# Performance work log

Measured on AMD Instinct MI355X. Metric: run time of the kernel, lower is better.

Reference implementation:

```python
import math
import jax, jax.numpy as jnp
import numpy as np

B, S, D, H = 4, 2048, 1024, 16
DH = D // H  # 64


def setup_inputs() -> dict:
    key = jax.random.key(0)
    k1, k2, k3 = jax.random.split(key, 3)
    x = jax.random.normal(k1, (B, S, D), dtype=jnp.float32)
    W_qkv = jax.random.normal(k2, (D, 3 * D), dtype=jnp.float32) * (1.0 / math.sqrt(D))
    b_qkv = jax.random.normal(k3, (3 * D,), dtype=jnp.float32) * 0.02
    return {"x": x, "W_qkv": W_qkv, "b_qkv": b_qkv}


def reference(x, W_qkv, b_qkv):
    b, s, d = x.shape
    qkv = x @ W_qkv + b_qkv                       # [B,S,3D]
    # Faithful to torch: view(B,S,H,3,D_h) -> interleaved per-head q/k/v split
    qkv = qkv.reshape(b, s, H, 3, DH)
    q = jnp.transpose(qkv[:, :, :, 0, :], (0, 2, 1, 3))  # [B,H,S,DH]
    k = jnp.transpose(qkv[:, :, :, 1, :], (0, 2, 1, 3))
    v = jnp.transpose(qkv[:, :, :, 2, :], (0, 2, 1, 3))
    scores = jnp.einsum('bhsd,bhtd->bhst', q, k) / math.sqrt(DH)  # [B,H,S,S]
    causal = jnp.triu(jnp.ones((s, s), dtype=bool), k=1)
    scores = jnp.where(causal, -jnp.inf, scores)
    weights = jax.nn.softmax(scores, axis=-1)
    # dropout is identity in eval/reference mode
    context = jnp.einsum('bhst,bhtd->bhsd', weights, v)  # [B,H,S,DH]
    return jnp.transpose(context, (0, 2, 1, 3)).reshape(b, s, d)
```

## Files before the change

kernel.cpp:

```cpp
#include <hip/hip_runtime.h>
#include <hip/hip_bf16.h>

#define Bz 4
#define Sz 2048
#define Dz 1024
#define Hz 16
#define DHz 64
#define Mz (Bz*Sz)
#define N3z (3*Dz)
#define Kz Dz

typedef short s16x8 __attribute__((ext_vector_type(8)));
typedef float f32x4 __attribute__((ext_vector_type(4)));
typedef unsigned short u16;

__device__ __forceinline__ u16 f2b(float f) {
  union { float f; unsigned u; } v; v.f = f;
  unsigned r = v.u + 0x7FFFu + ((v.u >> 16) & 1u);
  return (u16)(r >> 16);
}

__device__ __forceinline__ unsigned cvt_pk_bf16(float lo, float hi) {
  unsigned r;
  asm("v_cvt_pk_bf16_f32 %0, %1, %2" : "=v"(r) : "v"(lo), "v"(hi));
  return r;
}

__global__ __launch_bounds__(256) void cvt_x(const float* __restrict__ x,
                                             u16* __restrict__ xb) {
  int i = (blockIdx.x * 256 + threadIdx.x) * 4;
  float4 v = *reinterpret_cast<const float4*>(x + i);
  ushort4 o;
  o.x = f2b(v.x); o.y = f2b(v.y); o.z = f2b(v.z); o.w = f2b(v.w);
  *reinterpret_cast<ushort4*>(xb + i) = o;
}

__global__ __launch_bounds__(256) void transpose_w(const float* __restrict__ W,
                                                   u16* __restrict__ Wt) {
  __shared__ u16 t[32][33];
  int nb = blockIdx.x;
  int kb = blockIdx.y;
  int tx = threadIdx.x, ty = threadIdx.y;
#pragma unroll
  for (int j = 0; j < 4; ++j) {
    int k = kb * 32 + ty + j * 8;
    t[ty + j * 8][tx] = f2b(W[(size_t)k * N3z + nb * 32 + tx]);
  }
  __syncthreads();
#pragma unroll
  for (int j = 0; j < 4; ++j) {
    int n = nb * 32 + ty + j * 8;
    Wt[(size_t)n * Kz + kb * 32 + tx] = t[tx][ty + j * 8];
  }
}

#define BM 128
#define BN 128
#define BKs 64
#define QSCALE (0.125f * 1.44269504088896f)

__global__ __launch_bounds__(256) void qkv_gemm(
    const u16* __restrict__ A, const u16* __restrict__ Bt,
    const float* __restrict__ bias,
    u16* __restrict__ Qo, u16* __restrict__ Ko, u16* __restrict__ Vt) {
  __shared__ alignas(16) u16 As[BM * BKs];
  __shared__ alignas(16) u16 Bs[BN * BKs];
  const int tid = threadIdx.x;
  const int wid = tid >> 6, lane = tid & 63;
  const int wr = wid >> 1, wc = wid & 1;
  const int g = lane >> 4, lq = lane & 15;

  const int id = blockIdx.x + gridDim.x * blockIdx.y;
  const int xc = id & 7, rr = id >> 3;
  const int bx = xc * 8 + (rr & 7);
  const int by = rr >> 3;
  const int brow = bx * BM;
  const int bcol = by * BN;

  const int soff = (((lane & 7) ^ (lane >> 3))) * 8;

  f32x4 acc[4][4] = {};

  for (int kt = 0; kt < Kz; kt += BKs) {
#pragma unroll
    for (int c = 0; c < 4; ++c) {
      int row = (wid * 4 + c) * 8 + (lane >> 3);
      const u16* ga = A + (size_t)(brow + row) * Kz + kt + soff;
      __builtin_amdgcn_global_load_lds(
          (const __attribute__((address_space(1))) void*)ga,
          (__attribute__((address_space(3))) void*)&As[(wid * 4 + c) * 512],
          16, 0, 0);
      const u16* gb = Bt + (size_t)(bcol + row) * Kz + kt + soff;
      __builtin_amdgcn_global_load_lds(
          (const __attribute__((address_space(1))) void*)gb,
          (__attribute__((address_space(3))) void*)&Bs[(wid * 4 + c) * 512],
          16, 0, 0);
    }
    __syncthreads();

#pragma unroll
    for (int ks = 0; ks < 2; ++ks) {
      s16x8 af[4], bfr[4];
#pragma unroll
      for (int i = 0; i < 4; ++i) {
        int rowa = wr * 64 + i * 16 + lq;
        int rowb = wc * 64 + i * 16 + lq;
        int sl = ((ks * 4 + g) ^ (lq & 7)) << 4;
        af[i]  = *reinterpret_cast<const s16x8*>((const char*)As + rowa * 128 + sl);
        bfr[i] = *reinterpret_cast<const s16x8*>((const char*)Bs + rowb * 128 + sl);
      }
#pragma unroll
      for (int mi = 0; mi < 4; ++mi)
#pragma unroll
        for (int ni = 0; ni < 4; ++ni)
          acc[mi][ni] = __builtin_amdgcn_mfma_f32_16x16x32_bf16(af[mi], bfr[ni], acc[mi][ni], 0, 0, 0);
    }
    __syncthreads();
  }

#pragma unroll
  for (int ni = 0; ni < 4; ++ni) {
    int gcol = bcol + wc * 64 + ni * 16 + lq;
    int h = gcol / 192;
    int rem = gcol - h * 192;
    int tt = rem >> 6;
    int dh = rem & 63;
    float bv = bias[gcol];
    u16* dst = (tt == 0) ? Qo : (tt == 1) ? Ko : Vt;
    float scale = (tt == 0) ? QSCALE : 1.0f;
    bool isv = (tt == 2);
#pragma unroll
    for (int mi = 0; mi < 4; ++mi) {
#pragma unroll
      for (int r = 0; r < 4; ++r) {
        int grow = brow + wr * 64 + mi * 16 + g * 4 + r;
        int bb = grow >> 11;
        int ss = grow & 2047;
        float v = (acc[mi][ni][r] + bv) * scale;
        size_t off = isv ? ((((size_t)bb * Hz + h) * DHz + dh) * Sz + ss)
                         : ((((size_t)bb * Hz + h) * Sz + ss) * DHz + dh);
        dst[off] = f2b(v);
      }
    }
  }
}

__device__ __forceinline__ void attn_tile(
    const char* KsC, const char* VsC, int kv0, int q0w, int qrow,
    int g, int lq, int p, int cb, int sEven, int sOdd,
    const s16x8& qf0, const s16x8& qf1,
    f32x4 (&o)[4], float& m1, float& l1) {
  if (kv0 > q0w + 15) return;

  f32x4 z[4];
#pragma unroll
  for (int f = 0; f < 4; ++f) {
    int row = f * 16 + lq;
    s16x8 kb0 = *reinterpret_cast<const s16x8*>(KsC + row * 128 + ((g ^ (row & 7)) << 4));
    s16x8 kb1 = *reinterpret_cast<const s16x8*>(KsC + row * 128 + (((g + 4) ^ (row & 7)) << 4));
    f32x4 zz = {0.f, 0.f, 0.f, 0.f};
    zz = __builtin_amdgcn_mfma_f32_16x16x32_bf16(kb0, qf0, zz, 0, 0, 0);
    zz = __builtin_amdgcn_mfma_f32_16x16x32_bf16(kb1, qf1, zz, 0, 0, 0);
    z[f] = zz;
  }

  if (kv0 + 63 > q0w) {
#pragma unroll
    for (int f = 0; f < 4; ++f)
#pragma unroll
      for (int r = 0; r < 4; ++r) {
        int key = kv0 + f * 16 + g * 4 + r;
        if (key > qrow) z[f][r] = -1e30f;
      }
  }

  float pm = z[0][0];
#pragma unroll
  for (int f = 0; f < 4; ++f)
#pragma unroll
    for (int r = 0; r < 4; ++r) pm = fmaxf(pm, z[f][r]);
  pm = fmaxf(pm, __shfl_xor(pm, 16));
  pm = fmaxf(pm, __shfl_xor(pm, 32));

  if (!__all(pm <= m1 + 8.0f)) {
    float mn = fmaxf(m1, pm);
    float a = exp2f(m1 - mn);
    m1 = mn;
    l1 *= a;
    float a0 = __shfl(a, 4 * g + 0);
    float a1 = __shfl(a, 4 * g + 1);
    float a2 = __shfl(a, 4 * g + 2);
    float a3 = __shfl(a, 4 * g + 3);
#pragma unroll
    for (int ni = 0; ni < 4; ++ni) {
      o[ni][0] *= a0; o[ni][1] *= a1; o[ni][2] *= a2; o[ni][3] *= a3;
    }
  }

  float s = 0.f;
  unsigned w[4][2];
#pragma unroll
  for (int f = 0; f < 4; ++f) {
    float p0 = exp2f(z[f][0] - m1);
    float p1 = exp2f(z[f][1] - m1);
    float p2 = exp2f(z[f][2] - m1);
    float p3 = exp2f(z[f][3] - m1);
    s += (p0 + p1) + (p2 + p3);
    w[f][0] = cvt_pk_bf16(p0, p1);
    w[f][1] = cvt_pk_bf16(p2, p3);
  }
  s += __shfl_xor(s, 16);
  s += __shfl_xor(s, 32);
  l1 += s;

  int e0 = __shfl((int)(p ? w[1][0] : w[0][0]), sEven);
  int o0 = __shfl((int)(p ? w[0][0] : w[1][0]), sOdd);
  int e1 = __shfl((int)(p ? w[1][1] : w[0][1]), sEven);
  int o1 = __shfl((int)(p ? w[0][1] : w[1][1]), sOdd);
  int e2 = __shfl((int)(p ? w[3][0] : w[2][0]), sEven);
  int o2 = __shfl((int)(p ? w[2][0] : w[3][0]), sOdd);
  int e3 = __shfl((int)(p ? w[3][1] : w[2][1]), sEven);
  int o3 = __shfl((int)(p ? w[2][1] : w[3][1]), sOdd);
  union { int i[4]; s16x8 v; } A0, A1;
  A0.i[0] = cb ? o0 : e0;
  A0.i[2] = cb ? e0 : o0;
  A0.i[1] = cb ? o1 : e1;
  A0.i[3] = cb ? e1 : o1;
  A1.i[0] = cb ? o2 : e2;
  A1.i[2] = cb ? e2 : o2;
  A1.i[1] = cb ? o3 : e3;
  A1.i[3] = cb ? e3 : o3;

#pragma unroll
  for (int ni = 0; ni < 4; ++ni) {
    int row = ni * 16 + lq;
    s16x8 vb0 = *reinterpret_cast<const s16x8*>(VsC + row * 128 + ((g ^ (row & 7)) << 4));
    s16x8 vb1 = *reinterpret_cast<const s16x8*>(VsC + row * 128 + (((g + 4) ^ (row & 7)) << 4));
    o[ni] = __builtin_amdgcn_mfma_f32_16x16x32_bf16(A0.v, vb0, o[ni], 0, 0, 0);
    o[ni] = __builtin_amdgcn_mfma_f32_16x16x32_bf16(A1.v, vb1, o[ni], 0, 0, 0);
  }
}

__global__ __launch_bounds__(512, 4) void attn_kernel(
    const u16* __restrict__ Qg, const u16* __restrict__ Kg,
    const u16* __restrict__ Vtg, float* __restrict__ out) {
  __shared__ alignas(16) u16 Ks[2][64 * 64];
  __shared__ alignas(16) u16 Vs[2][64 * 64];

  const int tid = threadIdx.x;
  const int wid = tid >> 6, lane = tid & 63;
  const int g = lane >> 4, lq = lane & 15;

  const int id = blockIdx.x + 8 * blockIdx.y;
  const int xc = id & 7, rr = id >> 3;
  const int bh = xc * 8 + (rr & 7);
  const int qp = rr >> 3;

  const size_t base = (size_t)bh * Sz * DHz;
  const int b = bh >> 4, h = bh & 15;

  const int krow = tid >> 3;
  const int sswz = ((tid & 7) ^ (krow & 7)) * 8;

  const int p = g & 1;
  const int cb = g >> 1;
  const int sA = 32 * (g & 1) + lq;
  const int sB = sA + 16;
  const int sEven = cb ? sB : sA;
  const int sOdd  = cb ? sA : sB;

  const int qtA = qp, qtB = 15 - qp;
  const int q0wA = qtA * 128 + wid * 16;
  const int q0wB = qtB * 128 + wid * 16;
  const int qrowA = q0wA + lq, qrowB = q0wB + lq;
  const int ntA = 2 * qtA + 2, ntB = 2 * qtB + 2;

  s16x8 qfA0 = *reinterpret_cast<const s16x8*>(Qg + base + (size_t)qrowA * DHz + g * 8);
  s16x8 qfA1 = *reinterpret_cast<const s16x8*>(Qg + base + (size_t)qrowA * DHz + g * 8 + 32);
  s16x8 qfB0 = *reinterpret_cast<const s16x8*>(Qg + base + (size_t)qrowB * DHz + g * 8);
  s16x8 qfB1 = *reinterpret_cast<const s16x8*>(Qg + base + (size_t)qrowB * DHz + g * 8 + 32);

  f32x4 oA[4] = {}, oB[4] = {};
  float mA = -1e30f, lA = 0.f, mB = -1e30f, lB = 0.f;

  {
    const u16* gk = Kg + base + (size_t)krow * DHz + sswz;
    __builtin_amdgcn_global_load_lds(
        (const __attribute__((address_space(1))) void*)gk,
        (__attribute__((address_space(3))) void*)&Ks[0][wid * 512], 16, 0, 0);
    const u16* gv = Vtg + base + (size_t)krow * Sz + sswz;
    __builtin_amdgcn_global_load_lds(
        (const __attribute__((address_space(1))) void*)gv,
        (__attribute__((address_space(3))) void*)&Vs[0][wid * 512], 16, 0, 0);
  }
  __syncthreads();

  int cur = 0;
  for (int t = 0; t < ntB; ++t) {
    const int kv0 = t * 64;

    if (t + 1 < ntB) {
      const int nv0 = kv0 + 64;
      const u16* gk = Kg + base + (size_t)(nv0 + krow) * DHz + sswz;
      __builtin_amdgcn_global_load_lds(
          (const __attribute__((address_space(1))) void*)gk,
          (__attribute__((address_space(3))) void*)&Ks[cur ^ 1][wid * 512], 16, 0, 0);
      const u16* gv = Vtg + base + (size_t)krow * Sz + nv0 + sswz;
      __builtin_amdgcn_global_load_lds(
          (const __attribute__((address_space(1))) void*)gv,
          (__attribute__((address_space(3))) void*)&Vs[cur ^ 1][wid * 512], 16, 0, 0);
    }

    const char* KsC = (const char*)Ks[cur];
    const char* VsC = (const char*)Vs[cur];

    attn_tile(KsC, VsC, kv0, q0wB, qrowB, g, lq, p, cb, sEven, sOdd,
              qfB0, qfB1, oB, mB, lB);
    if (t < ntA)
      attn_tile(KsC, VsC, kv0, q0wA, qrowA, g, lq, p, cb, sEven, sOdd,
                qfA0, qfA1, oA, mA, lA);

    __syncthreads();
    cur ^= 1;
  }

#pragma unroll
  for (int half = 0; half < 2; ++half) {
    const int q0w = half ? q0wB : q0wA;
    f32x4* o = half ? oB : oA;
    float l1 = half ? lB : lA;
    float lr0 = __shfl(l1, 4 * g + 0);
    float lr1 = __shfl(l1, 4 * g + 1);
    float lr2 = __shfl(l1, 4 * g + 2);
    float lr3 = __shfl(l1, 4 * g + 3);
    float inv[4] = {1.0f / lr0, 1.0f / lr1, 1.0f / lr2, 1.0f / lr3};
#pragma unroll
    for (int r = 0; r < 4; ++r) {
      int s = q0w + g * 4 + r;
      float* op = out + (((size_t)b * Sz + s) * Hz + h) * DHz;
#pragma unroll
      for (int ni = 0; ni < 4; ++ni)
        op[ni * 16 + lq] = o[ni][r] * inv[r];
    }
  }
}

extern "C" void kernel_launch(void* const* d_in, const int* in_sizes, int n_in,
                              void* d_out, int out_size, void* d_ws, size_t ws_size,
                              hipStream_t stream) {
  const float* x    = (const float*)d_in[0];
  const float* W    = (const float*)d_in[1];
  const float* bias = (const float*)d_in[2];
  float* out = (float*)d_out;

  char* ws = (char*)d_ws;
  u16* xb = (u16*)(ws);
  u16* wt = (u16*)(ws + 16777216);
  u16* Qb = (u16*)(ws + 23068672);
  u16* Kb = (u16*)(ws + 39845888);
  u16* Vtb = (u16*)(ws + 56623104);

  cvt_x<<<8192, 256, 0, stream>>>(x, xb);
  transpose_w<<<dim3(96, 32), dim3(32, 8), 0, stream>>>(W, wt);
  qkv_gemm<<<dim3(Mz / BM, N3z / BN), 256, 0, stream>>>(xb, wt, bias, Qb, Kb, Vtb);
  attn_kernel<<<dim3(8, Bz * Hz), 512, 0, stream>>>(Qb, Kb, Vtb, out);
}
```

Before: 242.4 us.

## Fuse prep kernels, shrink GEMM K-tile, stage 128-key attention tiles

Merges the x conversion and W transpose kernels into one launch to save a launch. In the QKV GEMM it halves the K-tile to 32, drops the XOR LDS swizzle and the block-index remap, and uses plain row-major shared tiles. This may bring LDS bank conflicts and worse L2 locality. Attention now loads 128 keys per stage with double-buffered pairs of 64-key buffers, halving barrier count. It also unrolls the row-max reduction, but the A query tile is now processed on every stage even when fully masked, which adds redundant work.

New measurement: 234.8 us. -3.1%, faster.

```diff
diff --git a/kernel.cpp b/kernel.cpp
--- a/kernel.cpp
+++ b/kernel.cpp
@@ -26,37 +26,41 @@
   return r;
 }
 
-__global__ __launch_bounds__(256) void cvt_x(const float* __restrict__ x,
-                                             u16* __restrict__ xb) {
-  int i = (blockIdx.x * 256 + threadIdx.x) * 4;
-  float4 v = *reinterpret_cast<const float4*>(x + i);
-  ushort4 o;
-  o.x = f2b(v.x); o.y = f2b(v.y); o.z = f2b(v.z); o.w = f2b(v.w);
-  *reinterpret_cast<ushort4*>(xb + i) = o;
-}
-
-__global__ __launch_bounds__(256) void transpose_w(const float* __restrict__ W,
-                                                   u16* __restrict__ Wt) {
+__global__ __launch_bounds__(256) void prep(const float* __restrict__ x,
+                                            u16* __restrict__ xb,
+                                            const float* __restrict__ W,
+                                            u16* __restrict__ Wt) {
   __shared__ u16 t[32][33];
-  int nb = blockIdx.x;
-  int kb = blockIdx.y;
-  int tx = threadIdx.x, ty = threadIdx.y;
-#pragma unroll
-  for (int j = 0; j < 4; ++j) {
-    int k = kb * 32 + ty + j * 8;
-    t[ty + j * 8][tx] = f2b(W[(size_t)k * N3z + nb * 32 + tx]);
-  }
-  __syncthreads();
-#pragma unroll
-  for (int j = 0; j < 4; ++j) {
-    int n = nb * 32 + ty + j * 8;
-    Wt[(size_t)n * Kz + kb * 32 + tx] = t[tx][ty + j * 8];
+  const int bid = blockIdx.x;
+  const int tid = threadIdx.x;
+  if (bid < 8192) {
+    int i = (bid * 256 + tid) * 4;
+    float4 v = *reinterpret_cast<const float4*>(x + i);
+    ushort4 o;
+    o.x = f2b(v.x); o.y = f2b(v.y); o.z = f2b(v.z); o.w = f2b(v.w);
+    *reinterpret_cast<ushort4*>(xb + i) = o;
+  } else {
+    int id2 = bid - 8192;
+    int nb = id2 % 96;
+    int kb = id2 / 96;
+    int tx = tid & 31, ty = tid >> 5;
+#pragma unroll
+    for (int j = 0; j < 4; ++j) {
+      int k = kb * 32 + ty + j * 8;
+      t[ty + j * 8][tx] = f2b(W[(size_t)k * N3z + nb * 32 + tx]);
+    }
+    __syncthreads();
+#pragma unroll
+    for (int j = 0; j < 4; ++j) {
+      int n = nb * 32 + ty + j * 8;
+      Wt[(size_t)n * Kz + kb * 32 + tx] = t[tx][ty + j * 8];
+    }
   }
 }
 
 #define BM 128
 #define BN 128
-#define BKs 64
+#define BKs 32
 #define QSCALE (0.125f * 1.44269504088896f)
 
 __global__ __launch_bounds__(256) void qkv_gemm(
@@ -69,52 +73,40 @@
   const int wid = tid >> 6, lane = tid & 63;
   const int wr = wid >> 1, wc = wid & 1;
   const int g = lane >> 4, lq = lane & 15;
-
-  const int id = blockIdx.x + gridDim.x * blockIdx.y;
-  const int xc = id & 7, rr = id >> 3;
-  const int bx = xc * 8 + (rr & 7);
-  const int by = rr >> 3;
-  const int brow = bx * BM;
-  const int bcol = by * BN;
-
-  const int soff = (((lane & 7) ^ (lane >> 3))) * 8;
+  const int brow = blockIdx.x * BM;
+  const int bcol = blockIdx.y * BN;
 
   f32x4 acc[4][4] = {};
 
   for (int kt = 0; kt < Kz; kt += BKs) {
 #pragma unroll
-    for (int c = 0; c < 4; ++c) {
-      int row = (wid * 4 + c) * 8 + (lane >> 3);
-      const u16* ga = A + (size_t)(brow + row) * Kz + kt + soff;
+    for (int c = 0; c < 2; ++c) {
+      int row = (wid * 2 + c) * 16 + (lane >> 2);
+      int off = (lane & 3) * 8;
+      const u16* ga = A + (size_t)(brow + row) * Kz + kt + off;
       __builtin_amdgcn_global_load_lds(
           (const __attribute__((address_space(1))) void*)ga,
-          (__attribute__((address_space(3))) void*)&As[(wid * 4 + c) * 512],
+          (__attribute__((address_space(3))) void*)&As[(wid * 2 + c) * 512],
           16, 0, 0);
-      const u16* gb = Bt + (size_t)(bcol + row) * Kz + kt + soff;
+      const u16* gb = Bt + (size_t)(bcol + row) * Kz + kt + off;
       __builtin_amdgcn_global_load_lds(
           (const __attribute__((address_space(1))) void*)gb,
-          (__attribute__((address_space(3))) void*)&Bs[(wid * 4 + c) * 512],
+          (__attribute__((address_space(3))) void*)&Bs[(wid * 2 + c) * 512],
           16, 0, 0);
     }
     __syncthreads();
 
-#pragma unroll
-    for (int ks = 0; ks < 2; ++ks) {
-      s16x8 af[4], bfr[4];
-#pragma unroll
-      for (int i = 0; i < 4; ++i) {
-        int rowa = wr * 64 + i * 16 + lq;
-        int rowb = wc * 64 + i * 16 + lq;
-        int sl = ((ks * 4 + g) ^ (lq & 7)) << 4;
-        af[i]  = *reinterpret_cast<const s16x8*>((const char*)As + rowa * 128 + sl);
-        bfr[i] = *reinterpret_cast<const s16x8*>((const char*)Bs + rowb * 128 + sl);
-      }
-#pragma unroll
-      for (int mi = 0; mi < 4; ++mi)
-#pragma unroll
-        for (int ni = 0; ni < 4; ++ni)
-          acc[mi][ni] = __builtin_amdgcn_mfma_f32_16x16x32_bf16(af[mi], bfr[ni], acc[mi][ni], 0, 0, 0);
-    }
+    s16x8 af[4], bfr[4];
+#pragma unroll
+    for (int i = 0; i < 4; ++i) {
+      af[i]  = *reinterpret_cast<const s16x8*>(&As[(wr * 64 + i * 16 + lq) * BKs + g * 8]);
+      bfr[i] = *reinterpret_cast<const s16x8*>(&Bs[(wc * 64 + i * 16 + lq) * BKs + g * 8]);
+    }
+#pragma unroll
+    for (int mi = 0; mi < 4; ++mi)
+#pragma unroll
+      for (int ni = 0; ni < 4; ++ni)
+        acc[mi][ni] = __builtin_amdgcn_mfma_f32_16x16x32_bf16(af[mi], bfr[ni], acc[mi][ni], 0, 0, 0);
     __syncthreads();
   }
 
@@ -174,11 +166,15 @@
       }
   }
 
-  float pm = z[0][0];
-#pragma unroll
-  for (int f = 0; f < 4; ++f)
-#pragma unroll
-    for (int r = 0; r < 4; ++r) pm = fmaxf(pm, z[f][r]);
+  float pm;
+  pm = fmaxf(fmaxf(z[0][0], z[0][1]), z[0][2]);
+  pm = fmaxf(fmaxf(pm, z[0][3]), z[1][0]);
+  pm = fmaxf(fmaxf(pm, z[1][1]), z[1][2]);
+  pm = fmaxf(fmaxf(pm, z[1][3]), z[2][0]);
+  pm = fmaxf(fmaxf(pm, z[2][1]), z[2][2]);
+  pm = fmaxf(fmaxf(pm, z[2][3]), z[3][0]);
+  pm = fmaxf(fmaxf(pm, z[3][1]), z[3][2]);
+  pm = fmaxf(pm, z[3][3]);
   pm = fmaxf(pm, __shfl_xor(pm, 16));
   pm = fmaxf(pm, __shfl_xor(pm, 32));
 
@@ -244,8 +240,8 @@
 __global__ __launch_bounds__(512, 4) void attn_kernel(
     const u16* __restrict__ Qg, const u16* __restrict__ Kg,
     const u16* __restrict__ Vtg, float* __restrict__ out) {
-  __shared__ alignas(16) u16 Ks[2][64 * 64];
-  __shared__ alignas(16) u16 Vs[2][64 * 64];
+  __shared__ alignas(16) u16 Ks[2][2][64 * 64];
+  __shared__ alignas(16) u16 Vs[2][2][64 * 64];
 
   const int tid = threadIdx.x;
   const int wid = tid >> 6, lane = tid & 63;
@@ -273,7 +269,7 @@
   const int q0wA = qtA * 128 + wid * 16;
   const int q0wB = qtB * 128 + wid * 16;
   const int qrowA = q0wA + lq, qrowB = q0wB + lq;
-  const int ntA = 2 * qtA + 2, ntB = 2 * qtB + 2;
+  const int nT = qtB + 1;
 
   s16x8 qfA0 = *reinterpret_cast<const s16x8*>(Qg + base + (size_t)qrowA * DHz + g * 8);
   s16x8 qfA1 = *reinterpret_cast<const s16x8*>(Qg + base + (size_t)qrowA * DHz + g * 8 + 32);
@@ -283,42 +279,42 @@
   f32x4 oA[4] = {}, oB[4] = {};
   float mA = -1e30f, lA = 0.f, mB = -1e30f, lB = 0.f;
 
-  {
-    const u16* gk = Kg + base + (size_t)krow * DHz + sswz;
-    __builtin_amdgcn_global_load_lds(
-        (const __attribute__((address_space(1))) void*)gk,
-        (__attribute__((address_space(3))) void*)&Ks[0][wid * 512], 16, 0, 0);
-    const u16* gv = Vtg + base + (size_t)krow * Sz + sswz;
-    __builtin_amdgcn_global_load_lds(
-        (const __attribute__((address_space(1))) void*)gv,
-        (__attribute__((address_space(3))) void*)&Vs[0][wid * 512], 16, 0, 0);
-  }
+#define STAGE_T(bufb, TT) do {                                                  \
+    const u16* gk0 = Kg + base + (size_t)((TT) * 128 + krow) * DHz + sswz;      \
+    __builtin_amdgcn_global_load_lds(                                           \
+        (const __attribute__((address_space(1))) void*)gk0,                     \
+        (__attribute__((address_space(3))) void*)&Ks[bufb][0][wid * 512], 16, 0, 0); \
+    const u16* gk1 = Kg + base + (size_t)((TT) * 128 + 64 + krow) * DHz + sswz; \
+    __builtin_amdgcn_global_load_lds(                                           \
+        (const __attribute__((address_space(1))) void*)gk1,                     \
+        (__attribute__((address_space(3))) void*)&Ks[bufb][1][wid * 512], 16, 0, 0); \
+    const u16* gv0 = Vtg + base + (size_t)krow * Sz + (TT) * 128 + sswz;        \
+    __builtin_amdgcn_global_load_lds(                                           \
+        (const __attribute__((address_space(1))) void*)gv0,                     \
+        (__attribute__((address_space(3))) void*)&Vs[bufb][0][wid * 512], 16, 0, 0); \
+    const u16* gv1 = Vtg + base + (size_t)krow * Sz + (TT) * 128 + 64 + sswz;   \
+    __builtin_amdgcn_global_load_lds(                                           \
+        (const __attribute__((address_space(1))) void*)gv1,                     \
+        (__attribute__((address_space(3))) void*)&Vs[bufb][1][wid * 512], 16, 0, 0); \
+  } while (0)
+
+  STAGE_T(0, 0);
   __syncthreads();
 
   int cur = 0;
-  for (int t = 0; t < ntB; ++t) {
-    const int kv0 = t * 64;
-
-    if (t + 1 < ntB) {
-      const int nv0 = kv0 + 64;
-      const u16* gk = Kg + base + (size_t)(nv0 + krow) * DHz + sswz;
-      __builtin_amdgcn_global_load_lds(
-          (const __attribute__((address_space(1))) void*)gk,
-          (__attribute__((address_space(3))) void*)&Ks[cur ^ 1][wid * 512], 16, 0, 0);
-      const u16* gv = Vtg + base + (size_t)krow * Sz + nv0 + sswz;
-      __builtin_amdgcn_global_load_lds(
-          (const __attribute__((address_space(1))) void*)gv,
-          (__attribute__((address_space(3))) void*)&Vs[cur ^ 1][wid * 512], 16, 0, 0);
-    }
-
-    const char* KsC = (const char*)Ks[cur];
-    const char* VsC = (const char*)Vs[cur];
-
-    attn_tile(KsC, VsC, kv0, q0wB, qrowB, g, lq, p, cb, sEven, sOdd,
-              qfB0, qfB1, oB, mB, lB);
-    if (t < ntA)
+  for (int T = 0; T < nT; ++T) {
+    if (T + 1 < nT) STAGE_T(cur ^ 1, T + 1);
+
+#pragma unroll
+    for (int hh = 0; hh < 2; ++hh) {
+      const char* KsC = (const char*)Ks[cur][hh];
+      const char* VsC = (const char*)Vs[cur][hh];
+      const int kv0 = T * 128 + hh * 64;
+      attn_tile(KsC, VsC, kv0, q0wB, qrowB, g, lq, p, cb, sEven, sOdd,
+                qfB0, qfB1, oB, mB, lB);
       attn_tile(KsC, VsC, kv0, q0wA, qrowA, g, lq, p, cb, sEven, sOdd,
                 qfA0, qfA1, oA, mA, lA);
+    }
 
     __syncthreads();
     cur ^= 1;
@@ -360,8 +356,7 @@
   u16* Kb = (u16*)(ws + 39845888);
   u16* Vtb = (u16*)(ws + 56623104);
 
-  cvt_x<<<8192, 256, 0, stream>>>(x, xb);
-  transpose_w<<<dim3(96, 32), dim3(32, 8), 0, stream>>>(W, wt);
+  prep<<<8192 + 3072, 256, 0, stream>>>(x, xb, W, wt);
   qkv_gemm<<<dim3(Mz / BM, N3z / BN), 256, 0, stream>>>(xb, wt, bias, Qb, Kb, Vtb);
   attn_kernel<<<dim3(8, Bz * Hz), 512, 0, stream>>>(Qb, Kb, Vtb, out);
 }
```
